# Performance work log

Measured on AMD Instinct MI355X. Metric: run time of the kernel, lower is better.

Reference implementation:

```python
import jax, jax.numpy as jnp
import numpy as np

N_NODES = 50000
NEG_SLOPE = 0.01  # F.leaky_relu default


def setup_inputs() -> dict:
    key = jax.random.key(0)
    k1, k2, k3, k4, k5 = jax.random.split(key, 5)
    in_dim, out_dim, n_edges = 256, 64, 800000
    h = jax.random.normal(k1, (N_NODES, in_dim), dtype=jnp.float32)
    edge_src = jax.random.randint(k2, (n_edges,), 0, N_NODES, dtype=jnp.int32)
    edge_dst = jax.random.randint(k3, (n_edges,), 0, N_NODES, dtype=jnp.int32)
    W_fc = jax.random.normal(k4, (in_dim, out_dim), dtype=jnp.float32) / np.sqrt(in_dim)
    a_attn = jax.random.normal(k5, (2 * out_dim,), dtype=jnp.float32) / np.sqrt(2 * out_dim)
    return {"h": h, "edge_src": edge_src, "edge_dst": edge_dst, "W_fc": W_fc, "a_attn": a_attn}


def reference(h, edge_src, edge_dst, W_fc, a_attn):
    # z = fc(h)
    z = h @ W_fc                                   # [N, D]
    D = z.shape[1]
    # cat([z_src, z_dst]) @ a == z_src @ a_l + z_dst @ a_r (no edge concat materialized)
    a_l, a_r = a_attn[:D], a_attn[D:]
    s_l = z @ a_l                                  # [N]
    s_r = z @ a_r                                  # [N]
    e = s_l[edge_src] + s_r[edge_dst]              # [E]
    e = jnp.where(e > 0, e, NEG_SLOPE * e)         # leaky_relu
    # segment softmax over incoming edges of each dst node (DGL mailbox softmax)
    m = jax.ops.segment_max(e, edge_dst, num_segments=N_NODES)   # -inf for isolated nodes
    ex = jnp.exp(e - m[edge_dst])                  # [E]
    den = jax.ops.segment_sum(ex, edge_dst, num_segments=N_NODES)
    alpha = ex / den[edge_dst]                     # [E]
    # weighted neighbor aggregation: h_v = sum_{u->v} alpha * z_u
    msgs = alpha[:, None] * z[edge_src]            # [E, D]
    h_out = jax.ops.segment_sum(msgs, edge_dst, num_segments=N_NODES)  # [N, D]
    return h_out
```

## Files before the change

kernel.cpp:

```cpp
#include <hip/hip_runtime.h>

#define IN_DIM   256
#define OUT_DIM  64
#define NEG_SLOPE 0.01f
#define KPAD (IN_DIM + 8)
#define MAXBUCK 2048
#define CAP     1024
#define EPB     4096

typedef __attribute__((ext_vector_type(8))) short short8;
typedef __attribute__((ext_vector_type(4))) float f32x4;
typedef unsigned short ushort_t;

__device__ inline short f2bf(float f) {
    unsigned u = __float_as_uint(f);
    return (short)((u + 0x7FFF + ((u >> 16) & 1)) >> 16);
}
__device__ inline float bf2f(unsigned u16) { return __uint_as_float(u16 << 16); }

__global__ __launch_bounds__(256)
void prep_kernel(const float* __restrict__ W, short* __restrict__ Wt,
                 int* __restrict__ cnt, int nbuck)
{
    for (int i = threadIdx.x; i < nbuck; i += 256) cnt[i] = 0;
    for (int i = threadIdx.x; i < IN_DIM * OUT_DIM; i += 256) {
        const int k = i & (IN_DIM - 1);
        const int n = i >> 8;
        Wt[i] = f2bf(W[(size_t)k * OUT_DIM + n]);
    }
}

__global__ __launch_bounds__(256, 4)
void fused_kernel(const float* __restrict__ h, const short* __restrict__ Wt,
                  const float* __restrict__ a_attn,
                  ushort_t* __restrict__ z_bf, float* __restrict__ s_l,
                  float* __restrict__ s_r,
                  const int* __restrict__ esrc, const int* __restrict__ edst,
                  int* __restrict__ cnt, unsigned* __restrict__ perm,
                  int n_nodes, int n_edges, int nbuck, int ms_blocks)
{
    __shared__ union {
        short As[64 * KPAD];
        struct { int hist[MAXBUCK]; int cur[MAXBUCK]; } m;
    } sm;

    const int tid = threadIdx.x;

    if ((int)blockIdx.x < ms_blocks) {
        for (int i = tid; i < nbuck; i += 256) sm.m.hist[i] = 0;
        __syncthreads();
        const int base = blockIdx.x * EPB;
        unsigned pw[EPB / 256];
#pragma unroll
        for (int j = 0; j < EPB / 256; ++j) {
            const int i = base + j * 256 + tid;
            unsigned w = 0xFFFFFFFFu;
            if (i < n_edges) {
                const int d = edst[i];
                w = ((unsigned)d << 16) | (unsigned)esrc[i];
                atomicAdd(&sm.m.hist[d >> 5], 1);
            }
            pw[j] = w;
        }
        __syncthreads();
        for (int i = tid; i < nbuck; i += 256) {
            const int hv = sm.m.hist[i];
            if (hv) sm.m.cur[i] = i * CAP + atomicAdd(&cnt[i], hv);
        }
        __syncthreads();
#pragma unroll
        for (int j = 0; j < EPB / 256; ++j) {
            const unsigned w = pw[j];
            if (w != 0xFFFFFFFFu) {
                const int bk = (int)(w >> 21);
                const int pos = atomicAdd(&sm.m.cur[bk], 1);
                if (pos < (bk + 1) * CAP) perm[pos] = w;
            }
        }
        return;
    }

    const int wave = tid >> 6;
    const int lane = tid & 63;
    const int nbase = ((int)blockIdx.x - ms_blocks) * 64;

    for (int i = tid; i < 64 * (IN_DIM / 4); i += 256) {
        const int m  = i >> 6;
        const int k4 = i & 63;
        int node = nbase + m;
        if (node >= n_nodes) node = n_nodes - 1;
        const float4 h4 = *(const float4*)&h[(size_t)node * IN_DIM + k4 * 4];
        short* dp = &sm.As[m * KPAD + k4 * 4];
        dp[0] = f2bf(h4.x); dp[1] = f2bf(h4.y);
        dp[2] = f2bf(h4.z); dp[3] = f2bf(h4.w);
    }
    __syncthreads();

    f32x4 acc[4];
#pragma unroll
    for (int t = 0; t < 4; ++t) acc[t] = (f32x4){0.f, 0.f, 0.f, 0.f};

    const int col0 = lane & 15;
    const int quad = lane >> 4;
    const int mrow = wave * 16 + col0;
    const int kq   = quad * 8;

#pragma unroll
    for (int ks = 0; ks < IN_DIM / 32; ++ks) {
        const int kb = ks * 32 + kq;
        const short8 a = *(const short8*)&sm.As[mrow * KPAD + kb];
#pragma unroll
        for (int t = 0; t < 4; ++t) {
            const short8 b = *(const short8*)&Wt[(t * 16 + col0) * IN_DIM + kb];
            acc[t] = __builtin_amdgcn_mfma_f32_16x16x32_bf16(a, b, acc[t], 0, 0, 0);
        }
    }

    float al[4], ar[4];
#pragma unroll
    for (int t = 0; t < 4; ++t) {
        al[t] = a_attn[t * 16 + col0];
        ar[t] = a_attn[OUT_DIM + t * 16 + col0];
    }
#pragma unroll
    for (int r = 0; r < 4; ++r) {
        const int m = nbase + wave * 16 + quad * 4 + r;
        const bool live = m < n_nodes;
        float sl = 0.f, sr = 0.f;
#pragma unroll
        for (int t = 0; t < 4; ++t) {
            const float v = acc[t][r];
            if (live) z_bf[(size_t)m * OUT_DIM + t * 16 + col0] = (ushort_t)f2bf(v);
            sl += v * al[t];
            sr += v * ar[t];
        }
#pragma unroll
        for (int off = 1; off < 16; off <<= 1) {
            sl += __shfl_xor(sl, off, 16);
            sr += __shfl_xor(sr, off, 16);
        }
        if (live && col0 == 0) { s_l[m] = sl; s_r[m] = sr; }
    }
}

__global__ __launch_bounds__(512)
void gather_kernel(const unsigned* __restrict__ perm, const int* __restrict__ cnt,
                   const float* __restrict__ s_l, const float* __restrict__ s_r,
                   const ushort_t* __restrict__ z_bf, float* __restrict__ out,
                   int n_nodes)
{
    __shared__ unsigned eds[CAP];
    __shared__ ushort_t srcs[CAP];
    __shared__ int hist[32], starts[33], cur[32];

    const int tid = threadIdx.x;
    const int b   = blockIdx.x;
    int nE = cnt[b];
    if (nE > CAP) nE = CAP;

    if (tid < 32) hist[tid] = 0;
    __syncthreads();

    for (int i = tid; i < nE; i += 512) {
        const unsigned p = perm[(size_t)b * CAP + i];
        eds[i] = p;
        atomicAdd(&hist[(p >> 16) & 31], 1);
    }
    __syncthreads();

    if (tid < 32) {
        const int v = hist[tid];
        int inc = v;
#pragma unroll
        for (int off = 1; off < 32; off <<= 1) {
            const int u = __shfl_up(inc, off, 32);
            if (tid >= off) inc += u;
        }
        starts[tid + 1] = inc;
        cur[tid] = inc - v;
        if (tid == 0) starts[0] = 0;
    }
    __syncthreads();

    for (int i = tid; i < nE; i += 512) {
        const unsigned p = eds[i];
        const int pos = atomicAdd(&cur[(p >> 16) & 31], 1);
        srcs[pos] = (ushort_t)(p & 0xFFFFu);
    }
    __syncthreads();

    const int ld = tid >> 4;
    const int c  = tid & 15;
    const int d  = b * 32 + ld;
    if (d >= n_nodes) return;

    int k = starts[ld];
    const int ke = starts[ld + 1];
    const float srd = s_r[d];

    float a0 = 0.f, a1 = 0.f, a2 = 0.f, a3 = 0.f, den = 0.f;
    for (; k + 4 <= ke; k += 4) {
        const int s0 = srcs[k],     s1 = srcs[k + 1];
        const int s2 = srcs[k + 2], s3 = srcs[k + 3];
        const float l0 = s_l[s0], l1 = s_l[s1], l2 = s_l[s2], l3 = s_l[s3];
        const uint2 q0 = *(const uint2*)&z_bf[(size_t)s0 * OUT_DIM + c * 4];
        const uint2 q1 = *(const uint2*)&z_bf[(size_t)s1 * OUT_DIM + c * 4];
        const uint2 q2 = *(const uint2*)&z_bf[(size_t)s2 * OUT_DIM + c * 4];
        const uint2 q3 = *(const uint2*)&z_bf[(size_t)s3 * OUT_DIM + c * 4];
        float e0 = l0 + srd, e1 = l1 + srd, e2 = l2 + srd, e3 = l3 + srd;
        e0 = e0 > 0.f ? e0 : NEG_SLOPE * e0;
        e1 = e1 > 0.f ? e1 : NEG_SLOPE * e1;
        e2 = e2 > 0.f ? e2 : NEG_SLOPE * e2;
        e3 = e3 > 0.f ? e3 : NEG_SLOPE * e3;
        const float x0 = __expf(e0), x1 = __expf(e1);
        const float x2 = __expf(e2), x3 = __expf(e3);
        den += (x0 + x1) + (x2 + x3);
        a0 += x0 * bf2f(q0.x & 0xFFFFu) + x1 * bf2f(q1.x & 0xFFFFu)
            + x2 * bf2f(q2.x & 0xFFFFu) + x3 * bf2f(q3.x & 0xFFFFu);
        a1 += x0 * bf2f(q0.x >> 16)     + x1 * bf2f(q1.x >> 16)
            + x2 * bf2f(q2.x >> 16)     + x3 * bf2f(q3.x >> 16);
        a2 += x0 * bf2f(q0.y & 0xFFFFu) + x1 * bf2f(q1.y & 0xFFFFu)
            + x2 * bf2f(q2.y & 0xFFFFu) + x3 * bf2f(q3.y & 0xFFFFu);
        a3 += x0 * bf2f(q0.y >> 16)     + x1 * bf2f(q1.y >> 16)
            + x2 * bf2f(q2.y >> 16)     + x3 * bf2f(q3.y >> 16);
    }
    for (; k < ke; ++k) {
        const int s0 = srcs[k];
        float e0 = s_l[s0] + srd;
        e0 = e0 > 0.f ? e0 : NEG_SLOPE * e0;
        const float x0 = __expf(e0);
        const uint2 q0 = *(const uint2*)&z_bf[(size_t)s0 * OUT_DIM + c * 4];
        den += x0;
        a0 += x0 * bf2f(q0.x & 0xFFFFu);
        a1 += x0 * bf2f(q0.x >> 16);
        a2 += x0 * bf2f(q0.y & 0xFFFFu);
        a3 += x0 * bf2f(q0.y >> 16);
    }
    const float inv = den > 0.f ? 1.f / den : 0.f;
    float4 o;
    o.x = a0 * inv; o.y = a1 * inv; o.z = a2 * inv; o.w = a3 * inv;
    *(float4*)&out[(size_t)d * OUT_DIM + c * 4] = o;
}

extern "C" void kernel_launch(void* const* d_in, const int* in_sizes, int n_in,
                              void* d_out, int out_size, void* d_ws, size_t ws_size,
                              hipStream_t stream)
{
    const float* h        = (const float*)d_in[0];
    const int*   edge_src = (const int*)  d_in[1];
    const int*   edge_dst = (const int*)  d_in[2];
    const float* W        = (const float*)d_in[3];
    const float* a_attn   = (const float*)d_in[4];
    float*       out      = (float*)d_out;

    const int n_nodes = in_sizes[0] / IN_DIM;
    const int n_edges = in_sizes[1];
    const int nbuck   = (n_nodes + 31) >> 5;

    char* wsb = (char*)d_ws;
    short*    Wt   = (short*)wsb;
    size_t off = (size_t)IN_DIM * OUT_DIM * sizeof(short);
    ushort_t* z_bf = (ushort_t*)(wsb + off);
    off += (size_t)n_nodes * OUT_DIM * sizeof(ushort_t);
    float*    s_l  = (float*)(wsb + off);  off += (size_t)n_nodes * 4;
    float*    s_r  = (float*)(wsb + off);  off += (size_t)n_nodes * 4;
    int*      cnt  = (int*)(wsb + off);    off += ((size_t)nbuck * 4 + 15) & ~(size_t)15;
    unsigned* perm = (unsigned*)(wsb + off);

    const int ms_blocks   = (n_edges + EPB - 1) / EPB;
    const int gemm_blocks = (n_nodes + 63) / 64;

    prep_kernel<<<1, 256, 0, stream>>>(W, Wt, cnt, nbuck);
    fused_kernel<<<ms_blocks + gemm_blocks, 256, 0, stream>>>(
        h, Wt, a_attn, z_bf, s_l, s_r, edge_src, edge_dst, cnt, perm,
        n_nodes, n_edges, nbuck, ms_blocks);
    gather_kernel<<<nbuck, 512, 0, stream>>>(
        perm, cnt, s_l, s_r, z_bf, out, n_nodes);
}
```

Before: 137.8 us.

## Parallelize prep over 8 blocks, pack bf16 LDS stores, unroll gather by 8

The prep kernel now runs on 8 blocks instead of one, so zeroing the counters and transposing W to bf16 finish sooner. The GEMM staging packs four bf16 values into a single 64-bit LDS store instead of four 16-bit stores. The gather loop gains an 8-edge unrolled main loop that issues all index, score and z loads before the math, to keep more memory requests in flight. The cost is higher register pressure in the gather kernel and a slightly different summation order in the accumulation.

```diff
diff --git a/kernel.cpp b/kernel.cpp
--- a/kernel.cpp
+++ b/kernel.cpp
@@ -12,18 +12,20 @@
 typedef __attribute__((ext_vector_type(4))) float f32x4;
 typedef unsigned short ushort_t;
 
-__device__ inline short f2bf(float f) {
+__device__ inline unsigned f2bf_u(float f) {
     unsigned u = __float_as_uint(f);
-    return (short)((u + 0x7FFF + ((u >> 16) & 1)) >> 16);
-}
+    return (u + 0x7FFF + ((u >> 16) & 1)) >> 16;
+}
+__device__ inline short f2bf(float f) { return (short)f2bf_u(f); }
 __device__ inline float bf2f(unsigned u16) { return __uint_as_float(u16 << 16); }
 
 __global__ __launch_bounds__(256)
 void prep_kernel(const float* __restrict__ W, short* __restrict__ Wt,
                  int* __restrict__ cnt, int nbuck)
 {
-    for (int i = threadIdx.x; i < nbuck; i += 256) cnt[i] = 0;
-    for (int i = threadIdx.x; i < IN_DIM * OUT_DIM; i += 256) {
+    const int g = blockIdx.x * 256 + threadIdx.x;
+    for (int i = g; i < nbuck; i += 8 * 256) cnt[i] = 0;
+    for (int i = g; i < IN_DIM * OUT_DIM; i += 8 * 256) {
         const int k = i & (IN_DIM - 1);
         const int n = i >> 8;
         Wt[i] = f2bf(W[(size_t)k * OUT_DIM + n]);
@@ -90,9 +92,10 @@
         int node = nbase + m;
         if (node >= n_nodes) node = n_nodes - 1;
         const float4 h4 = *(const float4*)&h[(size_t)node * IN_DIM + k4 * 4];
-        short* dp = &sm.As[m * KPAD + k4 * 4];
-        dp[0] = f2bf(h4.x); dp[1] = f2bf(h4.y);
-        dp[2] = f2bf(h4.z); dp[3] = f2bf(h4.w);
+        uint2 p;
+        p.x = f2bf_u(h4.x) | (f2bf_u(h4.y) << 16);
+        p.y = f2bf_u(h4.z) | (f2bf_u(h4.w) << 16);
+        *(uint2*)&sm.As[m * KPAD + k4 * 4] = p;
     }
     __syncthreads();
 
@@ -199,43 +202,66 @@
     const float srd = s_r[d];
 
     float a0 = 0.f, a1 = 0.f, a2 = 0.f, a3 = 0.f, den = 0.f;
+
+    for (; k + 8 <= ke; k += 8) {
+        int   s[8];
+        float l[8];
+        uint2 q[8];
+#pragma unroll
+        for (int j = 0; j < 8; ++j) s[j] = srcs[k + j];
+#pragma unroll
+        for (int j = 0; j < 8; ++j) {
+            l[j] = s_l[s[j]];
+            q[j] = *(const uint2*)&z_bf[(size_t)s[j] * OUT_DIM + c * 4];
+        }
+#pragma unroll
+        for (int j = 0; j < 8; ++j) {
+            float e = l[j] + srd;
+            e = e > 0.f ? e : NEG_SLOPE * e;
+            const float x = __expf(e);
+            den += x;
+            a0 += x * bf2f(q[j].x & 0xFFFFu);
+            a1 += x * bf2f(q[j].x >> 16);
+            a2 += x * bf2f(q[j].y & 0xFFFFu);
+            a3 += x * bf2f(q[j].y >> 16);
+        }
+    }
     for (; k + 4 <= ke; k += 4) {
-        const int s0 = srcs[k],     s1 = srcs[k + 1];
-        const int s2 = srcs[k + 2], s3 = srcs[k + 3];
-        const float l0 = s_l[s0], l1 = s_l[s1], l2 = s_l[s2], l3 = s_l[s3];
-        const uint2 q0 = *(const uint2*)&z_bf[(size_t)s0 * OUT_DIM + c * 4];
-        const uint2 q1 = *(const uint2*)&z_bf[(size_t)s1 * OUT_DIM + c * 4];
-        const uint2 q2 = *(const uint2*)&z_bf[(size_t)s2 * OUT_DIM + c * 4];
-        const uint2 q3 = *(const uint2*)&z_bf[(size_t)s3 * OUT_DIM + c * 4];
-        float e0 = l0 + srd, e1 = l1 + srd, e2 = l2 + srd, e3 = l3 + srd;
-        e0 = e0 > 0.f ? e0 : NEG_SLOPE * e0;
-        e1 = e1 > 0.f ? e1 : NEG_SLOPE * e1;
-        e2 = e2 > 0.f ? e2 : NEG_SLOPE * e2;
-        e3 = e3 > 0.f ? e3 : NEG_SLOPE * e3;
-        const float x0 = __expf(e0), x1 = __expf(e1);
-        const float x2 = __expf(e2), x3 = __expf(e3);
-        den += (x0 + x1) + (x2 + x3);
-        a0 += x0 * bf2f(q0.x & 0xFFFFu) + x1 * bf2f(q1.x & 0xFFFFu)
-            + x2 * bf2f(q2.x & 0xFFFFu) + x3 * bf2f(q3.x & 0xFFFFu);
-        a1 += x0 * bf2f(q0.x >> 16)     + x1 * bf2f(q1.x >> 16)
-            + x2 * bf2f(q2.x >> 16)     + x3 * bf2f(q3.x >> 16);
-        a2 += x0 * bf2f(q0.y & 0xFFFFu) + x1 * bf2f(q1.y & 0xFFFFu)
-            + x2 * bf2f(q2.y & 0xFFFFu) + x3 * bf2f(q3.y & 0xFFFFu);
-        a3 += x0 * bf2f(q0.y >> 16)     + x1 * bf2f(q1.y >> 16)
-            + x2 * bf2f(q2.y >> 16)     + x3 * bf2f(q3.y >> 16);
+        int   s[4];
+        float l[4];
+        uint2 q[4];
+#pragma unroll
+        for (int j = 0; j < 4; ++j) s[j] = srcs[k + j];
+#pragma unroll
+        for (int j = 0; j < 4; ++j) {
+            l[j] = s_l[s[j]];
+            q[j] = *(const uint2*)&z_bf[(size_t)s[j] * OUT_DIM + c * 4];
+        }
+#pragma unroll
+        for (int j = 0; j < 4; ++j) {
+            float e = l[j] + srd;
+            e = e > 0.f ? e : NEG_SLOPE * e;
+            const float x = __expf(e);
+            den += x;
+            a0 += x * bf2f(q[j].x & 0xFFFFu);
+            a1 += x * bf2f(q[j].x >> 16);
+            a2 += x * bf2f(q[j].y & 0xFFFFu);
+            a3 += x * bf2f(q[j].y >> 16);
+        }
     }
     for (; k < ke; ++k) {
         const int s0 = srcs[k];
-        float e0 = s_l[s0] + srd;
-        e0 = e0 > 0.f ? e0 : NEG_SLOPE * e0;
-        const float x0 = __expf(e0);
+        float e = s_l[s0] + srd;
+        e = e > 0.f ? e : NEG_SLOPE * e;
+        const float x = __expf(e);
         const uint2 q0 = *(const uint2*)&z_bf[(size_t)s0 * OUT_DIM + c * 4];
-        den += x0;
-        a0 += x0 * bf2f(q0.x & 0xFFFFu);
-        a1 += x0 * bf2f(q0.x >> 16);
-        a2 += x0 * bf2f(q0.y & 0xFFFFu);
-        a3 += x0 * bf2f(q0.y >> 16);
-    }
+        den += x;
+        a0 += x * bf2f(q0.x & 0xFFFFu);
+        a1 += x * bf2f(q0.x >> 16);
+        a2 += x * bf2f(q0.y & 0xFFFFu);
+        a3 += x * bf2f(q0.y >> 16);
+    }
+
     const float inv = den > 0.f ? 1.f / den : 0.f;
     float4 o;
     o.x = a0 * inv; o.y = a1 * inv; o.z = a2 * inv; o.w = a3 * inv;
@@ -270,7 +296,7 @@
     const int ms_blocks   = (n_edges + EPB - 1) / EPB;
     const int gemm_blocks = (n_nodes + 63) / 64;
 
-    prep_kernel<<<1, 256, 0, stream>>>(W, Wt, cnt, nbuck);
+    prep_kernel<<<8, 256, 0, stream>>>(W, Wt, cnt, nbuck);
     fused_kernel<<<ms_blocks + gemm_blocks, 256, 0, stream>>>(
         h, Wt, a_attn, z_bf, s_l, s_r, edge_src, edge_dst, cnt, perm,
         n_nodes, n_edges, nbuck, ms_blocks);
```

Measured after the change: 133.9 us (median of 2 runs). 2.8% less time.
